# Kernel optimization log

Measured on AMD Instinct MI355X. Metric: run time of the kernel, lower is better.

## Reference

```python
import jax, jax.numpy as jnp
import numpy as np

B, D_IN, D_OUT, N_CTRL = 8192, 512, 512, 8

def setup_inputs() -> dict:
    key = jax.random.key(0)
    k1, k2, k3, k4 = jax.random.split(key, 4)
    inputs = jax.random.normal(k1, (B, D_IN), dtype=jnp.float32)
    # routing weights: positive soft blend coefficients, normalized per sample
    raw = jax.random.uniform(k2, (B, N_CTRL), dtype=jnp.float32)
    weights = raw / jnp.sum(raw, axis=-1, keepdims=True)
    w = jax.random.normal(k3, (N_CTRL, D_IN, D_OUT), dtype=jnp.float32) * 0.05
    b = jax.random.normal(k4, (N_CTRL, D_OUT), dtype=jnp.float32) * 0.05
    return {"inputs": inputs, "weights": weights, "w": w, "b": b}

def reference(inputs, weights, w, b):
    # Original math: w_p = einsum('ji,imk->jmk', weights, w)  [B, D_IN, D_OUT]
    #                out = squeeze(inputs[:, None, :] @ w_p) + weights @ b
    # Fused equivalent avoiding the [B, D_IN, D_OUT] intermediate:
    # run all n_control expert matmuls, then blend by routing weights.
    per_expert = jnp.einsum('bi,cio->cbo', inputs, w)       # [C, B, D_OUT]
    out = jnp.einsum('bc,cbo->bo', weights, per_expert)     # [B, D_OUT]
    out = out + weights @ b                                 # blended bias [B, D_OUT]
    return out
```

## Files before the change

kernel.cpp:

```cpp
#include <hip/hip_runtime.h>

#define B_   8192
#define DIN  512
#define DOUT 512
#define NC   8
#define NCD  (NC * DIN)
#define KSPL 4

typedef float  f32x4 __attribute__((ext_vector_type(4)));
typedef short  s16x8 __attribute__((ext_vector_type(8)));
typedef unsigned short u16x4 __attribute__((ext_vector_type(4)));
typedef unsigned int   u32x4 __attribute__((ext_vector_type(4)));

__device__ __forceinline__ unsigned short f2bf(float f) {
  unsigned u = __builtin_bit_cast(unsigned, f);
  u += 0x7fffu + ((u >> 16) & 1u);
  return (unsigned short)(u >> 16);
}
__device__ __forceinline__ float bf2f(unsigned short h) {
  unsigned u = ((unsigned)h) << 16;
  return __builtin_bit_cast(float, u);
}
__device__ __forceinline__ unsigned cvtpk(float lo, float hi) {
  unsigned r;
  asm("v_cvt_pk_bf16_f32 %0, %1, %2" : "=v"(r) : "v"(lo), "v"(hi));
  return r;
}
__device__ __forceinline__ void gl2lds16(const void* g, void* l) {
  __builtin_amdgcn_global_load_lds(
      (const __attribute__((address_space(1))) void*)g,
      (__attribute__((address_space(3))) void*)l, 16, 0, 0);
}

__global__ void pack_xw_k(const f32x4* __restrict__ x, u16x4* __restrict__ xb,
                          const float* __restrict__ w, unsigned short* __restrict__ Wt) {
  __shared__ float tile[64][65];
  const int tid = threadIdx.x;
  if (blockIdx.x < 4096) {
    int gid = blockIdx.x * 256 + tid;
    f32x4 v = x[gid];
    u16x4 o;
    o[0] = f2bf(v[0]); o[1] = f2bf(v[1]); o[2] = f2bf(v[2]); o[3] = f2bf(v[3]);
    xb[gid] = o;
    return;
  }
  const int idx = blockIdx.x - 4096;
  const int kt = idx & 63, nt = idx >> 6;
#pragma unroll
  for (int it = 0; it < 16; ++it) {
    int u = it * 256 + tid;
    int r = u >> 6, cc = u & 63;
    tile[r][cc] = w[(size_t)(kt * 64 + r) * DOUT + nt * 64 + cc];
  }
  __syncthreads();
#pragma unroll
  for (int it = 0; it < 16; ++it) {
    int u = it * 256 + tid;
    int rn = u >> 6, ck = u & 63;
    Wt[(size_t)(nt * 64 + rn) * NCD + kt * 64 + ck] = f2bf(tile[ck][rn]);
  }
}

__global__ __launch_bounds__(512, 2) void gemm_k(
    const unsigned short* __restrict__ xb,
    const unsigned short* __restrict__ Wt,
    const float* __restrict__ wt,
    unsigned short* __restrict__ part) {
  extern __shared__ char smem[];
  const int tid  = threadIdx.x;
  const int lane = tid & 63, wid = tid >> 6;
  const int wm = wid >> 2, wn = wid & 3;
  const int l15 = lane & 15, lhi = lane >> 4;

  const int n0   = blockIdx.x;
  const int by   = n0 >> 3;
  const int bx   = (n0 >> 2) & 1;
  const int ks   = n0 & 3;
  const int brow = by * 256, bcol = bx * 256;

  const int srow = tid >> 3, schunk = tid & 7;
  const unsigned short* gA = xb + (size_t)(brow + srow) * DIN + schunk * 8;
  const int adst_off = (schunk >> 2) * 16384 + srow * 64
                     + (((schunk & 3) ^ (srow & 3)) << 4);

  const int br = tid >> 2, bc = tid & 3;
  const unsigned short* gB0 = Wt + (size_t)(bcol + br) * NCD + ks * 1024
                                 + ((bc ^ (br & 3)) * 8);

  const float* wtp = wt + (size_t)(brow + srow) * NC + ks * 2;
  const float wtv0_0 = wtp[0],            wtv1_0 = wtp[1];
  const float wtv0_1 = wtp[64 * NC],      wtv1_1 = wtp[64 * NC + 1];
  const float wtv0_2 = wtp[128 * NC],     wtv1_2 = wtp[128 * NC + 1];
  const float wtv0_3 = wtp[192 * NC],     wtv1_3 = wtp[192 * NC + 1];

  f32x4 acc[8][4] = {};
  s16x8 areg0, areg1, areg2, areg3;
  s16x8 a[8], b[4];
  const int key    = (lhi ^ (l15 & 3)) << 4;
  const int abase2 = (wm * 128 + l15) * 64 + key;
  const int bbase2 = (wn * 64  + l15) * 64 + key;

#define STAGE_BH(H) {                                                        \
    const unsigned short* s_ = gB0 + ((H) >> 1) * 64 + ((H) & 1) * 32;       \
    char* l_ = smem + 65536 + ((H) & 3) * 16384 + tid * 16;                  \
    gl2lds16(s_, l_);                                                        \
    gl2lds16(s_ + (size_t)128 * NCD, l_ + 8192); }
#define LOAD_AREGS(kt) {                                                     \
    const unsigned short* s_ = gA + ((kt) & 7) * 64;                         \
    areg0 = *(const s16x8*)(s_);                                             \
    areg1 = *(const s16x8*)(s_ + (size_t) 64 * DIN);                         \
    areg2 = *(const s16x8*)(s_ + (size_t)128 * DIN);                         \
    areg3 = *(const s16x8*)(s_ + (size_t)192 * DIN); }
#define SCALE_STORE(AR, S, P, slotb) {                                       \
    u32x4 v_;                                                                \
    v_[0] = cvtpk(bf2f((unsigned short)AR[0]) * (S),                         \
                  bf2f((unsigned short)AR[1]) * (S));                        \
    v_[1] = cvtpk(bf2f((unsigned short)AR[2]) * (S),                         \
                  bf2f((unsigned short)AR[3]) * (S));                        \
    v_[2] = cvtpk(bf2f((unsigned short)AR[4]) * (S),                         \
                  bf2f((unsigned short)AR[5]) * (S));                        \
    v_[3] = cvtpk(bf2f((unsigned short)AR[6]) * (S),                         \
                  bf2f((unsigned short)AR[7]) * (S));                        \
    *(u32x4*)(smem + (slotb) + adst_off + (P) * 4096) = v_; }
#define SCALE_WRITE_ALL(e_, slotb) {                                         \
    SCALE_STORE(areg0, (e_) ? wtv1_0 : wtv0_0, 0, slotb);                    \
    SCALE_STORE(areg1, (e_) ? wtv1_1 : wtv0_1, 1, slotb);                    \
    SCALE_STORE(areg2, (e_) ? wtv1_2 : wtv0_2, 2, slotb);                    \
    SCALE_STORE(areg3, (e_) ? wtv1_3 : wtv0_3, 3, slotb); }
#define RD_HALF(aslotb, kk, bslot) {                                         \
    const char* pa_ = smem + (aslotb) + (kk) * 16384 + abase2;               \
    const char* pb_ = smem + 65536 + (bslot) * 16384 + bbase2;               \
    _Pragma("unroll") for (int m = 0; m < 8; ++m)                            \
      a[m] = *(const s16x8*)(pa_ + m * 1024);                                \
    _Pragma("unroll") for (int n = 0; n < 4; ++n)                            \
      b[n] = *(const s16x8*)(pb_ + n * 1024); }
#define MFMA_HALF()                                                          \
    _Pragma("unroll") for (int m = 0; m < 8; ++m)                            \
      _Pragma("unroll") for (int n = 0; n < 4; ++n)                          \
        acc[m][n] = __builtin_amdgcn_mfma_f32_16x16x32_bf16(                 \
            a[m], b[n], acc[m][n], 0, 0, 0);
#define BAR()   __builtin_amdgcn_s_barrier()
#define PRIO1() __builtin_amdgcn_s_setprio(1)
#define PRIO0() __builtin_amdgcn_s_setprio(0)
#define PIN()   asm volatile("" ::: "memory")
#define WAITV(N) asm volatile("s_waitcnt vmcnt(" #N ")" ::: "memory")
#define WAITL()  asm volatile("s_waitcnt lgkmcnt(0)" ::: "memory")

  PIN();
  LOAD_AREGS(0);
  PIN();
  STAGE_BH(0); STAGE_BH(1);
  WAITV(4);
  SCALE_WRITE_ALL(0, 0);
  LOAD_AREGS(1);
  WAITL();

  for (int t = 0; t < 16; ++t) {
    const int aslot = (t & 1) * 32768, oslot = 32768 - aslot;
    if (t < 15) { STAGE_BH(2 * t + 2); WAITV(8); }
    else        { WAITV(2); }
    BAR(); PIN();
    RD_HALF(aslot, 0, (2 * t) & 3);
    WAITL();
    __builtin_amdgcn_sched_barrier(0);
    PRIO1(); MFMA_HALF(); PRIO0();
    if (t < 15) { STAGE_BH(2 * t + 3); WAITV(8); }
    else        { WAITV(0); }
    BAR(); PIN();
    RD_HALF(aslot, 1, (2 * t + 1) & 3);
    if (t < 15) {
      WAITV(4);
      const int e = (t + 1) >> 3;
      SCALE_WRITE_ALL(e, oslot);
      if (t < 14) LOAD_AREGS(t + 2);
    }
    WAITL();
    __builtin_amdgcn_sched_barrier(0);
    PRIO1(); MFMA_HALF(); PRIO0();
  }

  __syncthreads();
  unsigned short* Cs = (unsigned short*)smem;
#pragma unroll
  for (int m = 0; m < 8; ++m)
#pragma unroll
    for (int n = 0; n < 4; ++n) {
      const int row = wm * 128 + m * 16 + (lane >> 4) * 4;
      const int col = wn * 64 + n * 16 + l15;
      f32x4 v = acc[m][n];
#pragma unroll
      for (int j = 0; j < 4; ++j)
        Cs[(row + j) * 264 + col] = f2bf(v[j]);
    }
  __syncthreads();
  unsigned short* pc = part + (size_t)ks * (B_ * DOUT) + (size_t)brow * DOUT + bcol;
#pragma unroll
  for (int it = 0; it < 16; ++it) {
    const int u = it * 512 + tid;
    const int row = u >> 5, cu = (u & 31) * 8;
    f32x4 v = *(const f32x4*)(Cs + row * 264 + cu);
    *(f32x4*)(pc + (size_t)row * DOUT + cu) = v;
  }
#undef STAGE_BH
#undef LOAD_AREGS
#undef SCALE_STORE
#undef SCALE_WRITE_ALL
#undef RD_HALF
#undef MFMA_HALF
#undef BAR
#undef PRIO1
#undef PRIO0
#undef PIN
#undef WAITV
#undef WAITL
}

__global__ void reduce_k(const unsigned short* __restrict__ part,
                         const float* __restrict__ wt,
                         const float* __restrict__ bias,
                         float* __restrict__ out) {
  int gid = blockIdx.x * 256 + threadIdx.x;
  int b = gid >> 7;
  int o4 = (gid & 127) << 2;
  float w8[8];
  *(f32x4*)w8       = *(const f32x4*)(wt + (size_t)b * NC);
  *(f32x4*)(w8 + 4) = *(const f32x4*)(wt + (size_t)b * NC + 4);
  f32x4 acc = {0.f, 0.f, 0.f, 0.f};
  const size_t off = (size_t)b * DOUT + o4;
#pragma unroll
  for (int s = 0; s < KSPL; ++s) {
    u16x4 p = *(const u16x4*)(part + (size_t)s * (B_ * DOUT) + off);
#pragma unroll
    for (int i = 0; i < 4; ++i) acc[i] += bf2f(p[i]);
  }
#pragma unroll
  for (int cc = 0; cc < NC; ++cc) {
    f32x4 bi = *(const f32x4*)(bias + cc * DOUT + o4);
#pragma unroll
    for (int i = 0; i < 4; ++i) acc[i] += w8[cc] * bi[i];
  }
  *(f32x4*)(out + off) = acc;
}

__global__ void bias_only_k(const float* __restrict__ wt,
                            const float* __restrict__ bias,
                            float* __restrict__ out) {
  int gid = blockIdx.x * 256 + threadIdx.x;
  int b = gid >> 7;
  int o4 = (gid & 127) << 2;
  float w8[8];
  *(f32x4*)w8       = *(const f32x4*)(wt + (size_t)b * NC);
  *(f32x4*)(w8 + 4) = *(const f32x4*)(wt + (size_t)b * NC + 4);
  f32x4 acc = {0.f, 0.f, 0.f, 0.f};
#pragma unroll
  for (int cc = 0; cc < NC; ++cc) {
    f32x4 bi = *(const f32x4*)(bias + cc * DOUT + o4);
#pragma unroll
    for (int i = 0; i < 4; ++i) acc[i] += w8[cc] * bi[i];
  }
  *(f32x4*)(out + (size_t)b * DOUT + o4) = acc;
}

extern "C" void kernel_launch(void* const* d_in, const int* in_sizes, int n_in,
                              void* d_out, int out_size, void* d_ws, size_t ws_size,
                              hipStream_t stream) {
  const float *x = nullptr, *wtc = nullptr, *w = nullptr, *bias = nullptr;
  for (int i = 0; i < n_in; ++i) {
    switch (in_sizes[i]) {
      case B_ * DIN:        x    = (const float*)d_in[i]; break;
      case B_ * NC:         wtc  = (const float*)d_in[i]; break;
      case NC * DIN * DOUT: w    = (const float*)d_in[i]; break;
      case NC * DOUT:       bias = (const float*)d_in[i]; break;
    }
  }
  float* out = (float*)d_out;

  const size_t XB_ELEMS   = (size_t)B_ * DIN;
  const size_t WT_ELEMS   = (size_t)DOUT * NCD;
  const size_t PART_ELEMS = (size_t)KSPL * B_ * DOUT;
  const size_t need = (XB_ELEMS + WT_ELEMS + PART_ELEMS) * sizeof(unsigned short);

  if (ws_size < need) {
    bias_only_k<<<(B_ * DOUT / 4) / 256, 256, 0, stream>>>(wtc, bias, out);
    return;
  }

  unsigned short* xb   = (unsigned short*)d_ws;
  unsigned short* Wt   = xb + XB_ELEMS;
  unsigned short* part = Wt + WT_ELEMS;

  const int GEMM_LDS = 256 * 264 * 2;
  (void)hipFuncSetAttribute((const void*)gemm_k,
                            hipFuncAttributeMaxDynamicSharedMemorySize, GEMM_LDS);

  pack_xw_k<<<4096 + 512, 256, 0, stream>>>((const f32x4*)x, (u16x4*)xb, w, Wt);
  gemm_k<<<256, 512, GEMM_LDS, stream>>>(xb, Wt, wtc, part);
  reduce_k<<<(B_ * DOUT / 4) / 256, 256, 0, stream>>>(part, wtc, bias, out);
}
```

Before: 65.11 us.

## Pre-pack W into MFMA fragment layout and load B directly to registers

The pack kernel now writes the bf16 expert weights in a fragment-ordered layout, so each lane's 16-byte B operand for the 16x16x32 MFMA sits contiguously in global memory. The GEMM no longer stages B through LDS via global_load_lds. It loads B fragments straight into registers, double-buffered across the two k-halves, and restructures the A tile in LDS to a 128-byte row stride with an 8-way XOR swizzle. This removes the B LDS traffic and some barriers, at the cost of more global/L2 traffic per wave, since B is no longer shared across the two wm waves, and higher register use.

```diff
diff --git a/kernel.cpp b/kernel.cpp
--- a/kernel.cpp
+++ b/kernel.cpp
@@ -26,14 +26,9 @@
   asm("v_cvt_pk_bf16_f32 %0, %1, %2" : "=v"(r) : "v"(lo), "v"(hi));
   return r;
 }
-__device__ __forceinline__ void gl2lds16(const void* g, void* l) {
-  __builtin_amdgcn_global_load_lds(
-      (const __attribute__((address_space(1))) void*)g,
-      (__attribute__((address_space(3))) void*)l, 16, 0, 0);
-}
 
 __global__ void pack_xw_k(const f32x4* __restrict__ x, u16x4* __restrict__ xb,
-                          const float* __restrict__ w, unsigned short* __restrict__ Wt) {
+                          const float* __restrict__ w, unsigned short* __restrict__ WtF) {
   __shared__ float tile[64][65];
   const int tid = threadIdx.x;
   if (blockIdx.x < 4096) {
@@ -45,25 +40,37 @@
     return;
   }
   const int idx = blockIdx.x - 4096;
-  const int kt = idx & 63, nt = idx >> 6;
+  const int kb = idx & 63, nb = idx >> 6;
+  const int e = kb >> 3, ktl = kb & 7;
 #pragma unroll
   for (int it = 0; it < 16; ++it) {
     int u = it * 256 + tid;
     int r = u >> 6, cc = u & 63;
-    tile[r][cc] = w[(size_t)(kt * 64 + r) * DOUT + nt * 64 + cc];
+    tile[r][cc] = w[(size_t)(e * 512 + ktl * 64 + r) * DOUT + nb * 64 + cc];
   }
   __syncthreads();
 #pragma unroll
-  for (int it = 0; it < 16; ++it) {
-    int u = it * 256 + tid;
-    int rn = u >> 6, ck = u & 63;
-    Wt[(size_t)(nt * 64 + rn) * NCD + kt * 64 + ck] = f2bf(tile[ck][rn]);
+  for (int it = 0; it < 2; ++it) {
+    int c = it * 256 + tid;
+    int n16l = c >> 7, kk = (c >> 6) & 1, l = c & 63;
+    int l15 = l & 15, lhi = l >> 4;
+    int col_in = n16l * 16 + l15;
+    int k_in   = kk * 32 + lhi * 8;
+    int n16    = nb * 4 + n16l;
+    u16x4 o0, o1;
+    o0[0] = f2bf(tile[k_in + 0][col_in]); o0[1] = f2bf(tile[k_in + 1][col_in]);
+    o0[2] = f2bf(tile[k_in + 2][col_in]); o0[3] = f2bf(tile[k_in + 3][col_in]);
+    o1[0] = f2bf(tile[k_in + 4][col_in]); o1[1] = f2bf(tile[k_in + 5][col_in]);
+    o1[2] = f2bf(tile[k_in + 6][col_in]); o1[3] = f2bf(tile[k_in + 7][col_in]);
+    size_t base = ((((size_t)e * 32 + n16) * 8 + ktl) * 2 + kk) * 512 + l * 8;
+    *(u16x4*)(WtF + base)     = o0;
+    *(u16x4*)(WtF + base + 4) = o1;
   }
 }
 
 __global__ __launch_bounds__(512, 2) void gemm_k(
     const unsigned short* __restrict__ xb,
-    const unsigned short* __restrict__ Wt,
+    const unsigned short* __restrict__ WtF,
     const float* __restrict__ wt,
     unsigned short* __restrict__ part) {
   extern __shared__ char smem[];
@@ -79,13 +86,15 @@
   const int brow = by * 256, bcol = bx * 256;
 
   const int srow = tid >> 3, schunk = tid & 7;
+  const int swz  = schunk ^ (srow & 7);
   const unsigned short* gA = xb + (size_t)(brow + srow) * DIN + schunk * 8;
-  const int adst_off = (schunk >> 2) * 16384 + srow * 64
-                     + (((schunk & 3) ^ (srow & 3)) << 4);
-
-  const int br = tid >> 2, bc = tid & 3;
-  const unsigned short* gB0 = Wt + (size_t)(bcol + br) * NCD + ks * 1024
-                                 + ((bc ^ (br & 3)) * 8);
+  const int adst_off = srow * 128 + swz * 16;
+
+  const unsigned short* bn0 = WtF + (size_t)(ks * 2) * 262144
+                                  + (size_t)(bx * 16 + wn * 4 + 0) * 8192 + lane * 8;
+  const unsigned short* bn1 = bn0 + 8192;
+  const unsigned short* bn2 = bn0 + 16384;
+  const unsigned short* bn3 = bn0 + 24576;
 
   const float* wtp = wt + (size_t)(brow + srow) * NC + ks * 2;
   const float wtv0_0 = wtp[0],            wtv1_0 = wtp[1];
@@ -95,16 +104,18 @@
 
   f32x4 acc[8][4] = {};
   s16x8 areg0, areg1, areg2, areg3;
-  s16x8 a[8], b[4];
-  const int key    = (lhi ^ (l15 & 3)) << 4;
-  const int abase2 = (wm * 128 + l15) * 64 + key;
-  const int bbase2 = (wn * 64  + l15) * 64 + key;
-
-#define STAGE_BH(H) {                                                        \
-    const unsigned short* s_ = gB0 + ((H) >> 1) * 64 + ((H) & 1) * 32;       \
-    char* l_ = smem + 65536 + ((H) & 3) * 16384 + tid * 16;                  \
-    gl2lds16(s_, l_);                                                        \
-    gl2lds16(s_ + (size_t)128 * NCD, l_ + 8192); }
+  s16x8 a[8], b0q[4], b1q[4];
+  const int x7    = l15 & 7;
+  const int pc0   = (lhi ^ x7) * 16;
+  const int pc1   = ((4 + lhi) ^ x7) * 16;
+  const int abase = (wm * 128 + l15) * 128;
+
+#define LOAD_B(BQ, et, ktl, kk) {                                            \
+    const size_t o_ = (size_t)(et) * 262144 + ((ktl) * 2 + (kk)) * 512;      \
+    BQ[0] = *(const s16x8*)(bn0 + o_);                                       \
+    BQ[1] = *(const s16x8*)(bn1 + o_);                                       \
+    BQ[2] = *(const s16x8*)(bn2 + o_);                                       \
+    BQ[3] = *(const s16x8*)(bn3 + o_); }
 #define LOAD_AREGS(kt) {                                                     \
     const unsigned short* s_ = gA + ((kt) & 7) * 64;                         \
     areg0 = *(const s16x8*)(s_);                                             \
@@ -121,62 +132,50 @@
                   bf2f((unsigned short)AR[5]) * (S));                        \
     v_[3] = cvtpk(bf2f((unsigned short)AR[6]) * (S),                         \
                   bf2f((unsigned short)AR[7]) * (S));                        \
-    *(u32x4*)(smem + (slotb) + adst_off + (P) * 4096) = v_; }
+    *(u32x4*)(smem + (slotb) + adst_off + (P) * 8192) = v_; }
 #define SCALE_WRITE_ALL(e_, slotb) {                                         \
     SCALE_STORE(areg0, (e_) ? wtv1_0 : wtv0_0, 0, slotb);                    \
     SCALE_STORE(areg1, (e_) ? wtv1_1 : wtv0_1, 1, slotb);                    \
     SCALE_STORE(areg2, (e_) ? wtv1_2 : wtv0_2, 2, slotb);                    \
     SCALE_STORE(areg3, (e_) ? wtv1_3 : wtv0_3, 3, slotb); }
-#define RD_HALF(aslotb, kk, bslot) {                                         \
-    const char* pa_ = smem + (aslotb) + (kk) * 16384 + abase2;               \
-    const char* pb_ = smem + 65536 + (bslot) * 16384 + bbase2;               \
+#define RD_A8(slotb, PC) {                                                   \
+    const char* pa_ = smem + (slotb) + abase + (PC);                         \
     _Pragma("unroll") for (int m = 0; m < 8; ++m)                            \
-      a[m] = *(const s16x8*)(pa_ + m * 1024);                                \
-    _Pragma("unroll") for (int n = 0; n < 4; ++n)                            \
-      b[n] = *(const s16x8*)(pb_ + n * 1024); }
-#define MFMA_HALF()                                                          \
+      a[m] = *(const s16x8*)(pa_ + m * 2048); }
+#define MFMA_HALF(BQ)                                                        \
     _Pragma("unroll") for (int m = 0; m < 8; ++m)                            \
       _Pragma("unroll") for (int n = 0; n < 4; ++n)                          \
         acc[m][n] = __builtin_amdgcn_mfma_f32_16x16x32_bf16(                 \
-            a[m], b[n], acc[m][n], 0, 0, 0);
+            a[m], BQ[n], acc[m][n], 0, 0, 0);
 #define BAR()   __builtin_amdgcn_s_barrier()
 #define PRIO1() __builtin_amdgcn_s_setprio(1)
 #define PRIO0() __builtin_amdgcn_s_setprio(0)
-#define PIN()   asm volatile("" ::: "memory")
-#define WAITV(N) asm volatile("s_waitcnt vmcnt(" #N ")" ::: "memory")
-#define WAITL()  asm volatile("s_waitcnt lgkmcnt(0)" ::: "memory")
-
-  PIN();
+#define SBAR0() __builtin_amdgcn_sched_barrier(0)
+#define WAITL() asm volatile("s_waitcnt lgkmcnt(0)" ::: "memory")
+
   LOAD_AREGS(0);
-  PIN();
-  STAGE_BH(0); STAGE_BH(1);
-  WAITV(4);
   SCALE_WRITE_ALL(0, 0);
   LOAD_AREGS(1);
+  LOAD_B(b0q, 0, 0, 0);
   WAITL();
+  BAR();
 
   for (int t = 0; t < 16; ++t) {
-    const int aslot = (t & 1) * 32768, oslot = 32768 - aslot;
-    if (t < 15) { STAGE_BH(2 * t + 2); WAITV(8); }
-    else        { WAITV(2); }
-    BAR(); PIN();
-    RD_HALF(aslot, 0, (2 * t) & 3);
-    WAITL();
-    __builtin_amdgcn_sched_barrier(0);
-    PRIO1(); MFMA_HALF(); PRIO0();
-    if (t < 15) { STAGE_BH(2 * t + 3); WAITV(8); }
-    else        { WAITV(0); }
-    BAR(); PIN();
-    RD_HALF(aslot, 1, (2 * t + 1) & 3);
+    const int ct = (t & 1) * 32768, ot = 32768 - ct;
+    const int ktl = t & 7, et = t >> 3;
+    RD_A8(ct, pc0);
+    LOAD_B(b1q, et, ktl, 1);
+    WAITL(); SBAR0();
+    PRIO1(); MFMA_HALF(b0q); PRIO0();
+    RD_A8(ct, pc1);
     if (t < 15) {
-      WAITV(4);
-      const int e = (t + 1) >> 3;
-      SCALE_WRITE_ALL(e, oslot);
+      SCALE_WRITE_ALL(((t + 1) >> 3), ot);
       if (t < 14) LOAD_AREGS(t + 2);
     }
-    WAITL();
-    __builtin_amdgcn_sched_barrier(0);
-    PRIO1(); MFMA_HALF(); PRIO0();
+    WAITL(); SBAR0();
+    PRIO1(); MFMA_HALF(b1q); PRIO0();
+    if (t < 15) LOAD_B(b0q, ((t + 1) >> 3), ((t + 1) & 7), 0);
+    BAR();
   }
 
   __syncthreads();
@@ -185,7 +184,7 @@
   for (int m = 0; m < 8; ++m)
 #pragma unroll
     for (int n = 0; n < 4; ++n) {
-      const int row = wm * 128 + m * 16 + (lane >> 4) * 4;
+      const int row = wm * 128 + m * 16 + lhi * 4;
       const int col = wn * 64 + n * 16 + l15;
       f32x4 v = acc[m][n];
 #pragma unroll
@@ -201,17 +200,16 @@
     f32x4 v = *(const f32x4*)(Cs + row * 264 + cu);
     *(f32x4*)(pc + (size_t)row * DOUT + cu) = v;
   }
-#undef STAGE_BH
+#undef LOAD_B
 #undef LOAD_AREGS
 #undef SCALE_STORE
 #undef SCALE_WRITE_ALL
-#undef RD_HALF
+#undef RD_A8
 #undef MFMA_HALF
 #undef BAR
 #undef PRIO1
 #undef PRIO0
-#undef PIN
-#undef WAITV
+#undef SBAR0
 #undef WAITL
 }
 
@@ -276,7 +274,7 @@
   float* out = (float*)d_out;
 
   const size_t XB_ELEMS   = (size_t)B_ * DIN;
-  const size_t WT_ELEMS   = (size_t)DOUT * NCD;
+  const size_t WT_ELEMS   = (size_t)NC * DIN * DOUT;
   const size_t PART_ELEMS = (size_t)KSPL * B_ * DOUT;
   const size_t need = (XB_ELEMS + WT_ELEMS + PART_ELEMS) * sizeof(unsigned short);
 
@@ -286,14 +284,14 @@
   }
 
   unsigned short* xb   = (unsigned short*)d_ws;
-  unsigned short* Wt   = xb + XB_ELEMS;
-  unsigned short* part = Wt + WT_ELEMS;
+  unsigned short* WtF  = xb + XB_ELEMS;
+  unsigned short* part = WtF + WT_ELEMS;
 
   const int GEMM_LDS = 256 * 264 * 2;
   (void)hipFuncSetAttribute((const void*)gemm_k,
                             hipFuncAttributeMaxDynamicSharedMemorySize, GEMM_LDS);
 
-  pack_xw_k<<<4096 + 512, 256, 0, stream>>>((const f32x4*)x, (u16x4*)xb, w, Wt);
-  gemm_k<<<256, 512, GEMM_LDS, stream>>>(xb, Wt, wtc, part);
+  pack_xw_k<<<4096 + 512, 256, 0, stream>>>((const f32x4*)x, (u16x4*)xb, w, WtF);
+  gemm_k<<<256, 512, GEMM_LDS, stream>>>(xb, WtF, wtc, part);
   reduce_k<<<(B_ * DOUT / 4) / 256, 256, 0, stream>>>(part, wtc, bias, out);
 }
```

Result: faster. 62.41 us, median of 2 (-4.1%).
